# Optimization experiments

Measured on AMD Instinct MI355X. Metric: run time of the kernel, lower is better.

## Reference

```python
import jax, jax.numpy as jnp
import numpy as np

BN_EPS = 1e-5
CLAMP = 1e-10


def _three_nn(q, p):
    # q: (B,N,3) query points, p: (B,M,3) reference points
    # returns dist (B,N,3) euclidean distance to 3 nearest, idx (B,N,3)
    d2 = (jnp.sum(q * q, -1)[:, :, None] + jnp.sum(p * p, -1)[:, None, :]
          - 2.0 * jnp.einsum('bnd,bmd->bnm', q, p))  # (B,N,M)
    neg_vals, idx = jax.lax.top_k(-d2, 3)
    dist = jnp.sqrt(jnp.maximum(-neg_vals, 1e-20))
    return dist, idx


def _gather(feats_t, idx):
    # feats_t: (B,M,C), idx: (B,N,3) -> (B,N,3,C)
    return jax.vmap(lambda f, i: f[i])(feats_t, idx)


def _conv_bn_relu(x, W, b, g, beta):
    # x: (B,Cin,N); 1x1 Conv1d + BatchNorm1d (training-mode batch stats) + relu
    y = jnp.einsum('oc,bcn->bon', W, x) + b[None, :, None]
    mean = jnp.mean(y, axis=(0, 2), keepdims=True)
    var = jnp.mean((y - mean) ** 2, axis=(0, 2), keepdims=True)
    y = (y - mean) * jax.lax.rsqrt(var + BN_EPS)
    y = y * g[None, :, None] + beta[None, :, None]
    return jax.nn.relu(y)


def setup_inputs() -> dict:
    key = jax.random.key(0)
    ks = jax.random.split(key, 10)
    B, N, M, C2, C1 = 4, 8192, 2048, 256, 128
    inp = {
        'xyz1': jax.random.normal(ks[0], (B, 3, N), jnp.float32),
        'xyz2': jax.random.normal(ks[1], (B, 3, M), jnp.float32),
        'norm1': jax.random.normal(ks[2], (B, 3, N), jnp.float32),
        'norm2': jax.random.normal(ks[3], (B, 3, M), jnp.float32),
        'points1': jax.random.normal(ks[4], (B, C1, N), jnp.float32),
        'points2': jax.random.normal(ks[5], (B, C2, M), jnp.float32),
        'W0': jax.random.normal(ks[6], (256, C2 + C1), jnp.float32) * 0.05,
        'b0': jax.random.normal(ks[7], (256,), jnp.float32) * 0.05,
        'g0': jnp.ones((256,), jnp.float32),
        'be0': jnp.zeros((256,), jnp.float32),
        'W1': jax.random.normal(ks[8], (128, 256), jnp.float32) * 0.05,
        'b1': jax.random.normal(ks[9], (128,), jnp.float32) * 0.05,
        'g1': jnp.ones((128,), jnp.float32),
        'be1': jnp.zeros((128,), jnp.float32),
    }
    return inp


def reference(xyz1, xyz2, norm1, norm2, points1, points2,
              W0, b0, g0, be0, W1, b1, g1, be1):
    B, _, N = xyz1.shape
    # 3-NN search
    dist, idx = _three_nn(jnp.transpose(xyz1, (0, 2, 1)),
                          jnp.transpose(xyz2, (0, 2, 1)))  # (B,N,3)
    # normal distance between query normals and gathered neighbor normals
    grouped_norm = _gather(jnp.transpose(norm2, (0, 2, 1)), idx)        # (B,N,3,3)
    diff = jnp.transpose(norm1, (0, 2, 1))[:, :, None, :] - grouped_norm
    norm_dist = jnp.sqrt(jnp.sum(diff * diff, -1))                       # (B,N,3)
    # distance weights
    recip_dist = 1.0 / jnp.maximum(dist, CLAMP)
    weight = recip_dist / jnp.sum(recip_dist, 2, keepdims=True)
    # normal weights
    recip_nd = 1.0 / jnp.maximum(norm_dist, CLAMP)
    norm_weight = recip_nd / jnp.sum(recip_nd, 2, keepdims=True)
    weight = weight * norm_weight                                        # (B,N,3)
    # three_interpolate: weighted gather of points2
    gathered_pts = _gather(jnp.transpose(points2, (0, 2, 1)), idx)       # (B,N,3,C)
    interpolated = jnp.einsum('bnkc,bnk->bcn', gathered_pts, weight)     # (B,C,N)
    new_points = jnp.concatenate([interpolated, points1], axis=1)        # (B,C+C1,N)
    new_points = _conv_bn_relu(new_points, W0, b0, g0, be0)
    new_points = _conv_bn_relu(new_points, W1, b1, g1, be1)
    return new_points
```

## Files before the change

### kernel.cpp

```cpp
#include <hip/hip_runtime.h>
#include <hip/hip_bf16.h>
#include <cstdint>
#include <cstddef>

static constexpr int BB   = 4;
static constexpr int NN   = 8192;
static constexpr int MM   = 2048;
static constexpr int C1   = 128;
static constexpr int C2   = 256;
static constexpr int CH0  = C2 + C1;
static constexpr int O0   = 256;
static constexpr int O1   = 128;
static constexpr int NCOL = BB * NN;
static constexpr float BN_EPS = 1e-5f;

using u16 = unsigned short;
typedef __attribute__((ext_vector_type(8))) short short8;
typedef __attribute__((ext_vector_type(4))) float f32x4;

static __device__ __forceinline__ float bf2f(u16 u) {
    union { unsigned int i; float f; } v; v.i = ((unsigned int)u) << 16; return v.f;
}
static __device__ __forceinline__ u16 f2bf(float f) {
    union { float f; unsigned int i; } v; v.f = f;
    unsigned int r = (v.i + 0x7fffu + ((v.i >> 16) & 1u)) >> 16;
    return (u16)r;
}

__global__ __launch_bounds__(256) void prep_kernel(const float* __restrict__ points2,
                                                   u16* __restrict__ p2T,
                                                   const float* __restrict__ points1,
                                                   u16* __restrict__ p1T,
                                                   const float* __restrict__ W0f,
                                                   u16* __restrict__ W0b,
                                                   const float* __restrict__ W1f,
                                                   u16* __restrict__ W1b) {
    __shared__ float tile[32][33];
    int id = blockIdx.x;
    int t  = threadIdx.x;
    if (id < 6144) {
        const float* in; u16* out; int R, C, b, c0, r0;
        if (id < 2048) {
            in = points2; out = p2T; R = C2; C = MM;
            b = id >> 9; int rem = id & 511;
            c0 = (rem & 63) * 32; r0 = (rem >> 6) * 32;
        } else {
            int id2 = id - 2048;
            in = points1; out = p1T; R = C1; C = NN;
            b = id2 >> 10; int rem = id2 & 1023;
            c0 = (rem & 255) * 32; r0 = (rem >> 8) * 32;
        }
        int tx = t & 31, ty = t >> 5;
        const float* pin = in + (size_t)b * R * C;
        u16* pout = out + (size_t)b * R * C;
#pragma unroll
        for (int j = 0; j < 4; ++j) {
            int r = ty + j * 8;
            tile[r][tx] = pin[(size_t)(r0 + r) * C + (c0 + tx)];
        }
        __syncthreads();
#pragma unroll
        for (int j = 0; j < 4; ++j) {
            int c = ty + j * 8;
            pout[(size_t)(c0 + c) * R + (r0 + tx)] = f2bf(tile[tx][c]);
        }
    } else {
        int i = (id - 6144) * 256 + t;
        if (i < O0 * CH0) W0b[i] = f2bf(W0f[i]);
        else {
            int i2 = i - O0 * CH0;
            if (i2 < O1 * O0) W1b[i2] = f2bf(W1f[i2]);
        }
    }
}

__global__ __launch_bounds__(256) void three_nn_kernel(const float* __restrict__ xyz1,
                                                       const float* __restrict__ xyz2,
                                                       const float* __restrict__ norm1,
                                                       const float* __restrict__ norm2,
                                                       int* __restrict__ idxOut,
                                                       float* __restrict__ wOut) {
#pragma clang fp contract(off)
    constexpr int CH = 1024;
    __shared__ float4 pts[CH];
    int b    = blockIdx.x >> 8;
    int nblk = blockIdx.x & 255;
    int t    = threadIdx.x;
    int j    = t & 7;

    int n = nblk * 32 + (t >> 3);
    const float* x1 = xyz1 + (size_t)b * 3 * NN;
    float qx = x1[n], qy = x1[NN + n], qz = x1[2 * NN + n];
    float qq = (qx * qx + qy * qy) + qz * qz;

    const float* x2 = xyz2 + (size_t)b * 3 * MM;

    float d0 = 3.4e38f, d1 = 3.4e38f, d2v = 3.4e38f;
    int   i0 = 0, i1 = 0, i2 = 0;

    for (int chunk = 0; chunk < MM / CH; ++chunk) {
        __syncthreads();
        for (int i = t; i < CH; i += 256) {
            int m = chunk * CH + i;
            float px = x2[m];
            float py = x2[MM + m];
            float pz = x2[2 * MM + m];
            float pp = (px * px + py * py) + pz * pz;
            pts[i] = make_float4(px, py, pz, pp);
        }
        __syncthreads();

#pragma unroll 8
        for (int s = 0; s < CH / 8; ++s) {
            int ml = s * 8 + j;
            float4 P = pts[ml];
            float qp = (qx * P.x + qy * P.y) + qz * P.z;
            float d  = (qq + P.w) - 2.0f * qp;
            if (d < d2v) {
                int m = chunk * CH + ml;
                if (d < d1) {
                    if (d < d0) { d2v = d1; i2 = i1; d1 = d0; i1 = i0; d0 = d; i0 = m; }
                    else        { d2v = d1; i2 = i1; d1 = d;  i1 = m; }
                } else          { d2v = d;  i2 = m; }
            }
        }
    }

#pragma unroll
    for (int k = 1; k <= 4; k <<= 1) {
        float e0 = __shfl_xor(d0, k, 64), e1 = __shfl_xor(d1, k, 64), e2 = __shfl_xor(d2v, k, 64);
        int   f0 = __shfl_xor(i0, k, 64), f1 = __shfl_xor(i1, k, 64), f2 = __shfl_xor(i2, k, 64);
        float ed[3] = {e0, e1, e2}; int ef[3] = {f0, f1, f2};
#pragma unroll
        for (int e = 0; e < 3; ++e) {
            float dd = ed[e]; int ff = ef[e];
            bool b2 = (dd < d2v) || (dd == d2v && ff < i2);
            if (b2) {
                bool b1 = (dd < d1) || (dd == d1 && ff < i1);
                if (b1) {
                    d2v = d1; i2 = i1;
                    bool b0 = (dd < d0) || (dd == d0 && ff < i0);
                    if (b0) { d1 = d0; i1 = i0; d0 = dd; i0 = ff; }
                    else    { d1 = dd; i1 = ff; }
                } else { d2v = dd; i2 = ff; }
            }
        }
    }

    if (j == 0) {
        float s0 = sqrtf(fmaxf(d0, 1e-20f));
        float s1 = sqrtf(fmaxf(d1, 1e-20f));
        float s2 = sqrtf(fmaxf(d2v, 1e-20f));
        float r0 = 1.0f / fmaxf(s0, 1e-10f);
        float r1 = 1.0f / fmaxf(s1, 1e-10f);
        float r2 = 1.0f / fmaxf(s2, 1e-10f);
        float rs = (r0 + r1) + r2;
        float w0 = r0 / rs, w1 = r1 / rs, w2 = r2 / rs;

        const float* nm1 = norm1 + (size_t)b * 3 * NN;
        const float* nm2 = norm2 + (size_t)b * 3 * MM;
        float ax = nm1[n], ay = nm1[NN + n], az = nm1[2 * NN + n];
        float nd[3]; int ii[3] = {i0, i1, i2};
#pragma unroll
        for (int k = 0; k < 3; ++k) {
            int ik = ii[k];
            float dx = ax - nm2[ik];
            float dy = ay - nm2[MM + ik];
            float dz = az - nm2[2 * MM + ik];
            nd[k] = sqrtf((dx * dx + dy * dy) + dz * dz);
        }
        float m0 = 1.0f / fmaxf(nd[0], 1e-10f);
        float m1 = 1.0f / fmaxf(nd[1], 1e-10f);
        float m2 = 1.0f / fmaxf(nd[2], 1e-10f);
        float ms = (m0 + m1) + m2;

        int col = b * NN + n;
        idxOut[col * 3 + 0] = i0;
        idxOut[col * 3 + 1] = i1;
        idxOut[col * 3 + 2] = i2;
        wOut[col * 3 + 0] = w0 * (m0 / ms);
        wOut[col * 3 + 1] = w1 * (m1 / ms);
        wOut[col * 3 + 2] = w2 * (m2 / ms);
    }
}

__global__ __launch_bounds__(256) void build_xT_kernel(const int* __restrict__ idx,
                                                       const float* __restrict__ w,
                                                       const u16* __restrict__ p2T,
                                                       const u16* __restrict__ p1T,
                                                       u16* __restrict__ xT) {
    int t  = threadIdx.x;
    int l  = t & 63;
    int wv = t >> 6;
    int col = blockIdx.x * 4 + wv;
    int b = col >> 13;
    int n = col & (NN - 1);
    int i0 = idx[col * 3 + 0], i1 = idx[col * 3 + 1], i2 = idx[col * 3 + 2];
    float w0 = w[col * 3 + 0], w1 = w[col * 3 + 1], w2 = w[col * 3 + 2];
    const u16* base = p2T + (size_t)b * MM * C2;

    union { uint2 v; u16 u[4]; } a0, a1, a2, o;
    a0.v = *(const uint2*)(base + (size_t)i0 * C2 + l * 4);
    a1.v = *(const uint2*)(base + (size_t)i1 * C2 + l * 4);
    a2.v = *(const uint2*)(base + (size_t)i2 * C2 + l * 4);
#pragma unroll
    for (int e = 0; e < 4; ++e)
        o.u[e] = f2bf(w0 * bf2f(a0.u[e]) + w1 * bf2f(a1.u[e]) + w2 * bf2f(a2.u[e]));
    *(uint2*)(xT + (size_t)col * CH0 + l * 4) = o.v;

    if (l < 32) {
        uint2 p = *(const uint2*)(p1T + ((size_t)b * NN + n) * C1 + l * 4);
        *(uint2*)(xT + (size_t)col * CH0 + C2 + l * 4) = p;
    }
}

template <int KDIM, int LDC, int COLT, bool FUSEB>
__global__ __launch_bounds__(256) void gemm_bt_kernel(const u16* __restrict__ A,
                                                      const u16* __restrict__ Bt,
                                                      u16* __restrict__ Ct,
                                                      const float* __restrict__ bias,
                                                      const float* __restrict__ redB,
                                                      const float* __restrict__ gB,
                                                      const float* __restrict__ beB,
                                                      float invN,
                                                      float* __restrict__ partials) {
    constexpr int KT  = KDIM / 64;
    constexpr int NI  = COLT / 32;
    constexpr int ASZ = 128 * 64;
    constexpr int BSZ = COLT * 64;
    __shared__ u16 smem[2 * ASZ + 2 * BSZ];
    __shared__ float sSc[FUSEB ? KDIM : 1];
    __shared__ float sSh[FUSEB ? KDIM : 1];

    int t   = threadIdx.x;
    int l   = t & 63;
    int wv  = t >> 6;
    int rl  = l >> 3;
    int cg  = ((l & 7) ^ rl) * 8;
    int mb0 = blockIdx.y * 128;
    int cb0 = blockIdx.x * COLT;
    int lm  = l & 15;
    int q   = l >> 4;
    int wm0 = (wv & 1) * 64;
    int wn0 = (wv >> 1) * (COLT / 2);

    const u16* Abase = A  + (size_t)mb0 * KDIM;
    const u16* Bbase = Bt + (size_t)cb0 * KDIM;

    if (FUSEB) {
        int by = t >> 7, chL = t & 127;
        const float* base = redB + (size_t)by * 8 * 256;
        float s = 0.f, s2 = 0.f;
#pragma unroll
        for (int i = 0; i < 8; ++i) {
            s  += base[i * 256 + chL];
            s2 += base[i * 256 + 128 + chL];
        }
        float mean = s * invN;
        float var  = fmaxf(s2 * invN - mean * mean, 0.f);
        float inv  = rsqrtf(var + BN_EPS);
        float sc   = gB[t] * inv;
        sSc[t] = sc;
        sSh[t] = beB[t] - mean * sc;
        __syncthreads();
    }

    auto stage = [&](int buf, int k0) {
#pragma unroll
        for (int iss = 0; iss < 4; ++iss) {
            int row = wv * 32 + iss * 8;
            const u16* g = Abase + (size_t)(row + rl) * KDIM + k0 + cg;
            __builtin_amdgcn_global_load_lds(
                (const __attribute__((address_space(1))) unsigned int*)g,
                (__attribute__((address_space(3))) unsigned int*)(&smem[buf * ASZ + row * 64]),
                16, 0, 0);
        }
        if (!FUSEB) {
#pragma unroll
            for (int iss = 0; iss < COLT / 32; ++iss) {
                int row = wv * (COLT / 4) + iss * 8;
                const u16* g = Bbase + (size_t)(row + rl) * KDIM + k0 + cg;
                __builtin_amdgcn_global_load_lds(
                    (const __attribute__((address_space(1))) unsigned int*)g,
                    (__attribute__((address_space(3))) unsigned int*)(&smem[2 * ASZ + buf * BSZ + row * 64]),
                    16, 0, 0);
            }
        } else {
            int row = t >> 2;
            int kc  = (t & 3) * 16;
            const u16* gp = Bbase + (size_t)row * KDIM + k0 + kc;
            union { uint4 v; u16 u[8]; } lo, hi;
            lo.v = *(const uint4*)gp;
            hi.v = *(const uint4*)(gp + 8);
#pragma unroll
            for (int e = 0; e < 8; ++e) {
                float f0 = bf2f(lo.u[e]);
                lo.u[e] = f2bf(fmaxf(f0 * sSc[k0 + kc + e] + sSh[k0 + kc + e], 0.f));
                float f1 = bf2f(hi.u[e]);
                hi.u[e] = f2bf(fmaxf(f1 * sSc[k0 + kc + 8 + e] + sSh[k0 + kc + 8 + e], 0.f));
            }
            int c0 = kc >> 3;
            u16* dstB = &smem[2 * ASZ + buf * BSZ + row * 64];
            *(uint4*)&dstB[((c0)     ^ (row & 7)) * 8] = lo.v;
            *(uint4*)&dstB[((c0 + 1) ^ (row & 7)) * 8] = hi.v;
        }
    };

    f32x4 acc[4][NI] = {};

    stage(0, 0);
    for (int kt = 0; kt < KT; ++kt) {
        __syncthreads();
        if (kt + 1 < KT) stage((kt + 1) & 1, (kt + 1) * 64);
        const u16* As = &smem[(kt & 1) * ASZ];
        const u16* Bs = &smem[2 * ASZ + (kt & 1) * BSZ];
#pragma unroll
        for (int ks = 0; ks < 2; ++ks) {
            int csw = ((ks * 4 + q) ^ (lm & 7)) * 8;
            short8 av[4], bv[NI];
#pragma unroll
            for (int mi = 0; mi < 4; ++mi)
                av[mi] = *(const short8*)&As[(wm0 + mi * 16 + lm) * 64 + csw];
#pragma unroll
            for (int ni = 0; ni < NI; ++ni)
                bv[ni] = *(const short8*)&Bs[(wn0 + ni * 16 + lm) * 64 + csw];
#pragma unroll
            for (int mi = 0; mi < 4; ++mi)
#pragma unroll
                for (int ni = 0; ni < NI; ++ni)
                    acc[mi][ni] = __builtin_amdgcn_mfma_f32_16x16x32_bf16(
                        av[mi], bv[ni], acc[mi][ni], 0, 0, 0);
        }
    }

    u16*   Cs   = smem;
    float* reds = (float*)&smem[COLT * 136];

    __syncthreads();
    if (t < 256) reds[t] = 0.f;
    __syncthreads();

#pragma unroll
    for (int mi = 0; mi < 4; ++mi) {
        int chL = wm0 + mi * 16 + q * 4;
        float bv4[4];
#pragma unroll
        for (int r = 0; r < 4; ++r) bv4[r] = bias[mb0 + chL + r];
        float s[4]  = {0.f, 0.f, 0.f, 0.f};
        float s2[4] = {0.f, 0.f, 0.f, 0.f};
#pragma unroll
        for (int ni = 0; ni < NI; ++ni) {
            int colL = wn0 + ni * 16 + lm;
            union { u16 u[4]; uint2 d; } pk;
#pragma unroll
            for (int r = 0; r < 4; ++r) {
                float v = acc[mi][ni][r] + bv4[r];
                s[r]  += v;
                s2[r] += v * v;
                pk.u[r] = f2bf(v);
            }
            *(uint2*)&Cs[colL * 136 + chL] = pk.d;
        }
#pragma unroll
        for (int r = 0; r < 4; ++r) {
            float a = s[r], b2 = s2[r];
#pragma unroll
            for (int off = 1; off < 16; off <<= 1) {
                a  += __shfl_xor(a, off, 64);
                b2 += __shfl_xor(b2, off, 64);
            }
            if (lm == 0) {
                atomicAdd(&reds[chL + r], a);
                atomicAdd(&reds[128 + chL + r], b2);
            }
        }
    }
    __syncthreads();

    for (int u = t; u < COLT * 2; u += 256) {
        int c = u >> 1, h = u & 1;
        const u16* src = &Cs[c * 136 + h * 64];
        u16* dst = Ct + (size_t)(cb0 + c) * LDC + mb0 + h * 64;
#pragma unroll
        for (int jj = 0; jj < 8; ++jj)
            *(uint4*)(dst + jj * 8) = *(const uint4*)(src + jj * 8);
    }
    partials[((size_t)blockIdx.y * gridDim.x + blockIdx.x) * 256 + t] = reds[t];
}

__global__ __launch_bounds__(256) void reduce_partials_kernel(const float* __restrict__ in,
                                                              float* __restrict__ out,
                                                              int chunk) {
    int t = threadIdx.x, r = blockIdx.x;
    const float* base = in + (size_t)r * chunk * 256;
    float s = 0.f;
#pragma unroll 8
    for (int i = 0; i < chunk; ++i) s += base[(size_t)i * 256 + t];
    out[(size_t)r * 256 + t] = s;
}

__global__ __launch_bounds__(256) void finalize_kernel(const u16* __restrict__ y1T,
                                                       const float* __restrict__ red1,
                                                       const float* __restrict__ g1,
                                                       const float* __restrict__ be1,
                                                       float invN,
                                                       float* __restrict__ out) {
    __shared__ float tile[64][129];
    __shared__ float sc[O1], sh[O1];
    int t  = threadIdx.x;
    int b  = blockIdx.y;
    int n0 = blockIdx.x * 64;

    if (t < O1) {
        float s = 0.f, s2 = 0.f;
#pragma unroll
        for (int i = 0; i < 16; ++i) {
            s  += red1[i * 256 + t];
            s2 += red1[i * 256 + 128 + t];
        }
        float mean = s * invN;
        float var  = fmaxf(s2 * invN - mean * mean, 0.f);
        float inv  = rsqrtf(var + BN_EPS);
        float scv  = g1[t] * inv;
        sc[t] = scv;
        sh[t] = be1[t] - mean * scv;
    }
    __syncthreads();

#pragma unroll
    for (int it = 0; it < 32; ++it) {
        int flat = it * 256 + t;
        int cl = flat >> 7;
        int c  = flat & 127;
        int col = b * NN + n0 + cl;
        float v = bf2f(y1T[(size_t)col * O1 + c]);
        tile[cl][c] = fmaxf(v * sc[c] + sh[c], 0.f);
    }
    __syncthreads();
#pragma unroll
    for (int it = 0; it < 32; ++it) {
        int flat = it * 256 + t;
        int c  = flat >> 6;
        int nl = flat & 63;
        out[(size_t)b * O1 * NN + (size_t)c * NN + n0 + nl] = tile[nl][c];
    }
}

extern "C" void kernel_launch(void* const* d_in, const int* in_sizes, int n_in,
                              void* d_out, int out_size, void* d_ws, size_t ws_size,
                              hipStream_t stream) {
    (void)in_sizes; (void)n_in; (void)out_size; (void)ws_size;

    const float* xyz1    = (const float*)d_in[0];
    const float* xyz2    = (const float*)d_in[1];
    const float* norm1   = (const float*)d_in[2];
    const float* norm2   = (const float*)d_in[3];
    const float* points1 = (const float*)d_in[4];
    const float* points2 = (const float*)d_in[5];
    const float* W0f     = (const float*)d_in[6];
    const float* b0      = (const float*)d_in[7];
    const float* g0      = (const float*)d_in[8];
    const float* be0     = (const float*)d_in[9];
    const float* W1f     = (const float*)d_in[10];
    const float* b1      = (const float*)d_in[11];
    const float* g1      = (const float*)d_in[12];
    const float* be1     = (const float*)d_in[13];
    float* out = (float*)d_out;

    char* w8 = (char*)d_ws;
    size_t off = 0;
    auto carve = [&](size_t bytes) { void* p = w8 + off; off += (bytes + 255) & ~(size_t)255; return p; };
    int*   idxW   = (int*)  carve((size_t)NCOL * 3 * sizeof(int));
    float* wW     = (float*)carve((size_t)NCOL * 3 * sizeof(float));
    u16*   p2T    = (u16*)  carve((size_t)BB * MM * C2 * 2);
    u16*   p1T    = (u16*)  carve((size_t)BB * NN * C1 * 2);
    u16*   W0b    = (u16*)  carve((size_t)O0 * CH0 * 2);
    u16*   W1b    = (u16*)  carve((size_t)O1 * O0 * 2);
    u16*   xT     = (u16*)  carve((size_t)NCOL * CH0 * 2);
    u16*   y0T    = (u16*)  carve((size_t)NCOL * O0 * 2);
    u16*   y1T    = (u16*)  carve((size_t)NCOL * O1 * 2);
    float* part0  = (float*)carve((size_t)1024 * 256 * sizeof(float));
    float* part1  = (float*)carve((size_t)512 * 256 * sizeof(float));
    float* red0   = (float*)carve((size_t)16 * 256 * sizeof(float));
    float* red1   = (float*)carve((size_t)16 * 256 * sizeof(float));

    const float invN = 1.0f / (float)NCOL;

    prep_kernel<<<6656, 256, 0, stream>>>(points2, p2T, points1, p1T,
                                          W0f, W0b, W1f, W1b);

    three_nn_kernel<<<BB * (NN / 32), 256, 0, stream>>>(xyz1, xyz2, norm1, norm2, idxW, wW);

    build_xT_kernel<<<NCOL / 4, 256, 0, stream>>>(idxW, wW, p2T, p1T, xT);

    gemm_bt_kernel<CH0, O0, 64, false><<<dim3(NCOL / 64, O0 / 128), 256, 0, stream>>>(
        W0b, xT, y0T, b0, nullptr, nullptr, nullptr, invN, part0);
    reduce_partials_kernel<<<16, 256, 0, stream>>>(part0, red0, 64);

    gemm_bt_kernel<O0, O1, 64, true><<<dim3(NCOL / 64, O1 / 128), 256, 0, stream>>>(
        W1b, y0T, y1T, b1, red0, g0, be0, invN, part1);
    reduce_partials_kernel<<<16, 256, 0, stream>>>(part1, red1, 32);

    finalize_kernel<<<dim3(NN / 64, BB), 256, 0, stream>>>(y1T, red1, g1, be1, invN, out);
}
```

Measured before the change: 205.7 us.

## Fuse interpolation gather into first GEMM and process two queries per thread in 3-NN

```diff
diff --git a/kernel.cpp b/kernel.cpp
--- a/kernel.cpp
+++ b/kernel.cpp
@@ -83,20 +83,36 @@
 #pragma clang fp contract(off)
     constexpr int CH = 1024;
     __shared__ float4 pts[CH];
-    int b    = blockIdx.x >> 8;
-    int nblk = blockIdx.x & 255;
+    int b    = blockIdx.x >> 7;
+    int nblk = blockIdx.x & 127;
     int t    = threadIdx.x;
     int j    = t & 7;
 
-    int n = nblk * 32 + (t >> 3);
+    int n0 = nblk * 64 + (t >> 3) * 2;
+    int n1 = n0 + 1;
     const float* x1 = xyz1 + (size_t)b * 3 * NN;
-    float qx = x1[n], qy = x1[NN + n], qz = x1[2 * NN + n];
-    float qq = (qx * qx + qy * qy) + qz * qz;
+    float qxa = x1[n0], qya = x1[NN + n0], qza = x1[2 * NN + n0];
+    float qxb = x1[n1], qyb = x1[NN + n1], qzb = x1[2 * NN + n1];
+    float qqa = (qxa * qxa + qya * qya) + qza * qza;
+    float qqb = (qxb * qxb + qyb * qyb) + qzb * qzb;
 
     const float* x2 = xyz2 + (size_t)b * 3 * MM;
 
-    float d0 = 3.4e38f, d1 = 3.4e38f, d2v = 3.4e38f;
-    int   i0 = 0, i1 = 0, i2 = 0;
+    float da0 = 3.4e38f, da1 = 3.4e38f, da2 = 3.4e38f;
+    int   ia0 = 0, ia1 = 0, ia2 = 0;
+    float db0 = 3.4e38f, db1 = 3.4e38f, db2 = 3.4e38f;
+    int   ib0 = 0, ib1 = 0, ib2 = 0;
+
+    auto ins = [](float d, int m, float& e0, float& e1, float& e2,
+                  int& f0, int& f1, int& f2) {
+        bool m0 = d < e0, m1 = d < e1, m2 = d < e2;
+        e2 = m1 ? e1 : (m2 ? d : e2);
+        f2 = m1 ? f1 : (m2 ? m : f2);
+        e1 = m0 ? e0 : (m1 ? d : e1);
+        f1 = m0 ? f0 : (m1 ? m : f1);
+        e0 = m0 ? d : e0;
+        f0 = m0 ? m : f0;
+    };
 
     for (int chunk = 0; chunk < MM / CH; ++chunk) {
         __syncthreads();
@@ -110,113 +126,90 @@
         }
         __syncthreads();
 
-#pragma unroll 8
+#pragma unroll 4
         for (int s = 0; s < CH / 8; ++s) {
             int ml = s * 8 + j;
             float4 P = pts[ml];
-            float qp = (qx * P.x + qy * P.y) + qz * P.z;
-            float d  = (qq + P.w) - 2.0f * qp;
-            if (d < d2v) {
-                int m = chunk * CH + ml;
-                if (d < d1) {
-                    if (d < d0) { d2v = d1; i2 = i1; d1 = d0; i1 = i0; d0 = d; i0 = m; }
-                    else        { d2v = d1; i2 = i1; d1 = d;  i1 = m; }
-                } else          { d2v = d;  i2 = m; }
-            }
-        }
-    }
-
-#pragma unroll
-    for (int k = 1; k <= 4; k <<= 1) {
-        float e0 = __shfl_xor(d0, k, 64), e1 = __shfl_xor(d1, k, 64), e2 = __shfl_xor(d2v, k, 64);
-        int   f0 = __shfl_xor(i0, k, 64), f1 = __shfl_xor(i1, k, 64), f2 = __shfl_xor(i2, k, 64);
-        float ed[3] = {e0, e1, e2}; int ef[3] = {f0, f1, f2};
-#pragma unroll
-        for (int e = 0; e < 3; ++e) {
-            float dd = ed[e]; int ff = ef[e];
-            bool b2 = (dd < d2v) || (dd == d2v && ff < i2);
-            if (b2) {
-                bool b1 = (dd < d1) || (dd == d1 && ff < i1);
-                if (b1) {
-                    d2v = d1; i2 = i1;
-                    bool b0 = (dd < d0) || (dd == d0 && ff < i0);
-                    if (b0) { d1 = d0; i1 = i0; d0 = dd; i0 = ff; }
-                    else    { d1 = dd; i1 = ff; }
-                } else { d2v = dd; i2 = ff; }
-            }
-        }
-    }
+            int m = chunk * CH + ml;
+            float qpa = (qxa * P.x + qya * P.y) + qza * P.z;
+            float da  = (qqa + P.w) - 2.0f * qpa;
+            ins(da, m, da0, da1, da2, ia0, ia1, ia2);
+            float qpb = (qxb * P.x + qyb * P.y) + qzb * P.z;
+            float db  = (qqb + P.w) - 2.0f * qpb;
+            ins(db, m, db0, db1, db2, ib0, ib1, ib2);
+        }
+    }
+
+    auto merge = [&](float& e0, float& e1, float& e2, int& f0, int& f1, int& f2) {
+#pragma unroll
+        for (int k = 1; k <= 4; k <<= 1) {
+            float g0 = __shfl_xor(e0, k, 64), g1 = __shfl_xor(e1, k, 64), g2 = __shfl_xor(e2, k, 64);
+            int   h0 = __shfl_xor(f0, k, 64), h1 = __shfl_xor(f1, k, 64), h2 = __shfl_xor(f2, k, 64);
+            float ed[3] = {g0, g1, g2}; int ef[3] = {h0, h1, h2};
+#pragma unroll
+            for (int e = 0; e < 3; ++e) {
+                float dd = ed[e]; int ff = ef[e];
+                bool b2 = (dd < e2) || (dd == e2 && ff < f2);
+                if (b2) {
+                    bool b1 = (dd < e1) || (dd == e1 && ff < f1);
+                    if (b1) {
+                        e2 = e1; f2 = f1;
+                        bool b0 = (dd < e0) || (dd == e0 && ff < f0);
+                        if (b0) { e1 = e0; f1 = f0; e0 = dd; f0 = ff; }
+                        else    { e1 = dd; f1 = ff; }
+                    } else { e2 = dd; f2 = ff; }
+                }
+            }
+        }
+    };
+    merge(da0, da1, da2, ia0, ia1, ia2);
+    merge(db0, db1, db2, ib0, ib1, ib2);
 
     if (j == 0) {
-        float s0 = sqrtf(fmaxf(d0, 1e-20f));
-        float s1 = sqrtf(fmaxf(d1, 1e-20f));
-        float s2 = sqrtf(fmaxf(d2v, 1e-20f));
-        float r0 = 1.0f / fmaxf(s0, 1e-10f);
-        float r1 = 1.0f / fmaxf(s1, 1e-10f);
-        float r2 = 1.0f / fmaxf(s2, 1e-10f);
-        float rs = (r0 + r1) + r2;
-        float w0 = r0 / rs, w1 = r1 / rs, w2 = r2 / rs;
-
         const float* nm1 = norm1 + (size_t)b * 3 * NN;
         const float* nm2 = norm2 + (size_t)b * 3 * MM;
-        float ax = nm1[n], ay = nm1[NN + n], az = nm1[2 * NN + n];
-        float nd[3]; int ii[3] = {i0, i1, i2};
-#pragma unroll
-        for (int k = 0; k < 3; ++k) {
-            int ik = ii[k];
-            float dx = ax - nm2[ik];
-            float dy = ay - nm2[MM + ik];
-            float dz = az - nm2[2 * MM + ik];
-            nd[k] = sqrtf((dx * dx + dy * dy) + dz * dz);
-        }
-        float m0 = 1.0f / fmaxf(nd[0], 1e-10f);
-        float m1 = 1.0f / fmaxf(nd[1], 1e-10f);
-        float m2 = 1.0f / fmaxf(nd[2], 1e-10f);
-        float ms = (m0 + m1) + m2;
-
-        int col = b * NN + n;
-        idxOut[col * 3 + 0] = i0;
-        idxOut[col * 3 + 1] = i1;
-        idxOut[col * 3 + 2] = i2;
-        wOut[col * 3 + 0] = w0 * (m0 / ms);
-        wOut[col * 3 + 1] = w1 * (m1 / ms);
-        wOut[col * 3 + 2] = w2 * (m2 / ms);
-    }
-}
-
-__global__ __launch_bounds__(256) void build_xT_kernel(const int* __restrict__ idx,
-                                                       const float* __restrict__ w,
-                                                       const u16* __restrict__ p2T,
-                                                       const u16* __restrict__ p1T,
-                                                       u16* __restrict__ xT) {
-    int t  = threadIdx.x;
-    int l  = t & 63;
-    int wv = t >> 6;
-    int col = blockIdx.x * 4 + wv;
-    int b = col >> 13;
-    int n = col & (NN - 1);
-    int i0 = idx[col * 3 + 0], i1 = idx[col * 3 + 1], i2 = idx[col * 3 + 2];
-    float w0 = w[col * 3 + 0], w1 = w[col * 3 + 1], w2 = w[col * 3 + 2];
-    const u16* base = p2T + (size_t)b * MM * C2;
-
-    union { uint2 v; u16 u[4]; } a0, a1, a2, o;
-    a0.v = *(const uint2*)(base + (size_t)i0 * C2 + l * 4);
-    a1.v = *(const uint2*)(base + (size_t)i1 * C2 + l * 4);
-    a2.v = *(const uint2*)(base + (size_t)i2 * C2 + l * 4);
-#pragma unroll
-    for (int e = 0; e < 4; ++e)
-        o.u[e] = f2bf(w0 * bf2f(a0.u[e]) + w1 * bf2f(a1.u[e]) + w2 * bf2f(a2.u[e]));
-    *(uint2*)(xT + (size_t)col * CH0 + l * 4) = o.v;
-
-    if (l < 32) {
-        uint2 p = *(const uint2*)(p1T + ((size_t)b * NN + n) * C1 + l * 4);
-        *(uint2*)(xT + (size_t)col * CH0 + C2 + l * 4) = p;
-    }
-}
-
-template <int KDIM, int LDC, int COLT, bool FUSEB>
+        auto emit = [&](int n, float e0, float e1, float e2, int f0, int f1, int f2) {
+            float s0 = sqrtf(fmaxf(e0, 1e-20f));
+            float s1 = sqrtf(fmaxf(e1, 1e-20f));
+            float s2 = sqrtf(fmaxf(e2, 1e-20f));
+            float r0 = 1.0f / fmaxf(s0, 1e-10f);
+            float r1 = 1.0f / fmaxf(s1, 1e-10f);
+            float r2 = 1.0f / fmaxf(s2, 1e-10f);
+            float rs = (r0 + r1) + r2;
+            float w0 = r0 / rs, w1 = r1 / rs, w2 = r2 / rs;
+            float ax = nm1[n], ay = nm1[NN + n], az = nm1[2 * NN + n];
+            float nd[3]; int ii[3] = {f0, f1, f2};
+#pragma unroll
+            for (int k = 0; k < 3; ++k) {
+                int ik = ii[k];
+                float dx = ax - nm2[ik];
+                float dy = ay - nm2[MM + ik];
+                float dz = az - nm2[2 * MM + ik];
+                nd[k] = sqrtf((dx * dx + dy * dy) + dz * dz);
+            }
+            float m0 = 1.0f / fmaxf(nd[0], 1e-10f);
+            float m1 = 1.0f / fmaxf(nd[1], 1e-10f);
+            float m2 = 1.0f / fmaxf(nd[2], 1e-10f);
+            float ms = (m0 + m1) + m2;
+            int col = b * NN + n;
+            idxOut[col * 3 + 0] = f0;
+            idxOut[col * 3 + 1] = f1;
+            idxOut[col * 3 + 2] = f2;
+            wOut[col * 3 + 0] = w0 * (m0 / ms);
+            wOut[col * 3 + 1] = w1 * (m1 / ms);
+            wOut[col * 3 + 2] = w2 * (m2 / ms);
+        };
+        emit(n0, da0, da1, da2, ia0, ia1, ia2);
+        emit(n1, db0, db1, db2, ib0, ib1, ib2);
+    }
+}
+
+template <int KDIM, int LDC, int COLT, int MODE>
 __global__ __launch_bounds__(256) void gemm_bt_kernel(const u16* __restrict__ A,
                                                       const u16* __restrict__ Bt,
+                                                      const u16* __restrict__ p1T,
+                                                      const int* __restrict__ idx,
+                                                      const float* __restrict__ w,
                                                       u16* __restrict__ Ct,
                                                       const float* __restrict__ bias,
                                                       const float* __restrict__ redB,
@@ -229,8 +222,8 @@
     constexpr int ASZ = 128 * 64;
     constexpr int BSZ = COLT * 64;
     __shared__ u16 smem[2 * ASZ + 2 * BSZ];
-    __shared__ float sSc[FUSEB ? KDIM : 1];
-    __shared__ float sSh[FUSEB ? KDIM : 1];
+    __shared__ float sSc[MODE == 1 ? KDIM : 1];
+    __shared__ float sSh[MODE == 1 ? KDIM : 1];
 
     int t   = threadIdx.x;
     int l   = t & 63;
@@ -244,10 +237,18 @@
     int wm0 = (wv & 1) * 64;
     int wn0 = (wv >> 1) * (COLT / 2);
 
-    const u16* Abase = A  + (size_t)mb0 * KDIM;
-    const u16* Bbase = Bt + (size_t)cb0 * KDIM;
-
-    if (FUSEB) {
+    const u16* Abase = A + (size_t)mb0 * KDIM;
+
+    int vi0 = 0, vi1 = 0, vi2 = 0;
+    float vw0 = 0.f, vw1 = 0.f, vw2 = 0.f;
+    const u16* p2base = nullptr;
+    if (MODE == 2) {
+        int colg = cb0 + (t >> 2);
+        vi0 = idx[colg * 3 + 0]; vi1 = idx[colg * 3 + 1]; vi2 = idx[colg * 3 + 2];
+        vw0 = w[colg * 3 + 0];   vw1 = w[colg * 3 + 1];   vw2 = w[colg * 3 + 2];
+        p2base = Bt + (size_t)(cb0 >> 13) * MM * C2;
+    }
+    if (MODE == 1) {
         int by = t >> 7, chL = t & 127;
         const float* base = redB + (size_t)by * 8 * 256;
         float s = 0.f, s2 = 0.f;
@@ -275,20 +276,20 @@
                 (__attribute__((address_space(3))) unsigned int*)(&smem[buf * ASZ + row * 64]),
                 16, 0, 0);
         }
-        if (!FUSEB) {
+        if (MODE == 0) {
 #pragma unroll
             for (int iss = 0; iss < COLT / 32; ++iss) {
                 int row = wv * (COLT / 4) + iss * 8;
-                const u16* g = Bbase + (size_t)(row + rl) * KDIM + k0 + cg;
+                const u16* g = Bt + (size_t)(cb0 + row + rl) * KDIM + k0 + cg;
                 __builtin_amdgcn_global_load_lds(
                     (const __attribute__((address_space(1))) unsigned int*)g,
                     (__attribute__((address_space(3))) unsigned int*)(&smem[2 * ASZ + buf * BSZ + row * 64]),
                     16, 0, 0);
             }
-        } else {
+        } else if (MODE == 1) {
             int row = t >> 2;
             int kc  = (t & 3) * 16;
-            const u16* gp = Bbase + (size_t)row * KDIM + k0 + kc;
+            const u16* gp = Bt + (size_t)(cb0 + row) * KDIM + k0 + kc;
             union { uint4 v; u16 u[8]; } lo, hi;
             lo.v = *(const uint4*)gp;
             hi.v = *(const uint4*)(gp + 8);
@@ -303,6 +304,38 @@
             u16* dstB = &smem[2 * ASZ + buf * BSZ + row * 64];
             *(uint4*)&dstB[((c0)     ^ (row & 7)) * 8] = lo.v;
             *(uint4*)&dstB[((c0 + 1) ^ (row & 7)) * 8] = hi.v;
+        } else {
+            if (k0 < C2) {
+                int row = t >> 2;
+                int kc  = (t & 3) * 16;
+                const u16* bp = p2base + k0 + kc;
+                const u16* r0p = bp + (size_t)vi0 * C2;
+                const u16* r1p = bp + (size_t)vi1 * C2;
+                const u16* r2p = bp + (size_t)vi2 * C2;
+                union { uint4 v; u16 u[8]; } x0, x1, x2, y0, y1, y2, lo, hi;
+                x0.v = *(const uint4*)r0p; y0.v = *(const uint4*)(r0p + 8);
+                x1.v = *(const uint4*)r1p; y1.v = *(const uint4*)(r1p + 8);
+                x2.v = *(const uint4*)r2p; y2.v = *(const uint4*)(r2p + 8);
+#pragma unroll
+                for (int e = 0; e < 8; ++e) {
+                    lo.u[e] = f2bf(vw0 * bf2f(x0.u[e]) + vw1 * bf2f(x1.u[e]) + vw2 * bf2f(x2.u[e]));
+                    hi.u[e] = f2bf(vw0 * bf2f(y0.u[e]) + vw1 * bf2f(y1.u[e]) + vw2 * bf2f(y2.u[e]));
+                }
+                int c0 = kc >> 3;
+                u16* dstB = &smem[2 * ASZ + buf * BSZ + row * 64];
+                *(uint4*)&dstB[((c0)     ^ (row & 7)) * 8] = lo.v;
+                *(uint4*)&dstB[((c0 + 1) ^ (row & 7)) * 8] = hi.v;
+            } else {
+#pragma unroll
+                for (int iss = 0; iss < COLT / 32; ++iss) {
+                    int row = wv * (COLT / 4) + iss * 8;
+                    const u16* g = p1T + (size_t)(cb0 + row + rl) * C1 + (k0 - C2) + cg;
+                    __builtin_amdgcn_global_load_lds(
+                        (const __attribute__((address_space(1))) unsigned int*)g,
+                        (__attribute__((address_space(3))) unsigned int*)(&smem[2 * ASZ + buf * BSZ + row * 64]),
+                        16, 0, 0);
+                }
+            }
         }
     };
 
@@ -476,7 +509,6 @@
     u16*   p1T    = (u16*)  carve((size_t)BB * NN * C1 * 2);
     u16*   W0b    = (u16*)  carve((size_t)O0 * CH0 * 2);
     u16*   W1b    = (u16*)  carve((size_t)O1 * O0 * 2);
-    u16*   xT     = (u16*)  carve((size_t)NCOL * CH0 * 2);
     u16*   y0T    = (u16*)  carve((size_t)NCOL * O0 * 2);
     u16*   y1T    = (u16*)  carve((size_t)NCOL * O1 * 2);
     float* part0  = (float*)carve((size_t)1024 * 256 * sizeof(float));
@@ -489,16 +521,14 @@
     prep_kernel<<<6656, 256, 0, stream>>>(points2, p2T, points1, p1T,
                                           W0f, W0b, W1f, W1b);
 
-    three_nn_kernel<<<BB * (NN / 32), 256, 0, stream>>>(xyz1, xyz2, norm1, norm2, idxW, wW);
-
-    build_xT_kernel<<<NCOL / 4, 256, 0, stream>>>(idxW, wW, p2T, p1T, xT);
-
-    gemm_bt_kernel<CH0, O0, 64, false><<<dim3(NCOL / 64, O0 / 128), 256, 0, stream>>>(
-        W0b, xT, y0T, b0, nullptr, nullptr, nullptr, invN, part0);
+    three_nn_kernel<<<BB * (NN / 64), 256, 0, stream>>>(xyz1, xyz2, norm1, norm2, idxW, wW);
+
+    gemm_bt_kernel<CH0, O0, 64, 2><<<dim3(NCOL / 64, O0 / 128), 256, 0, stream>>>(
+        W0b, p2T, p1T, idxW, wW, y0T, b0, nullptr, nullptr, nullptr, invN, part0);
     reduce_partials_kernel<<<16, 256, 0, stream>>>(part0, red0, 64);
 
-    gemm_bt_kernel<O0, O1, 64, true><<<dim3(NCOL / 64, O1 / 128), 256, 0, stream>>>(
-        W1b, y0T, y1T, b1, red0, g0, be0, invN, part1);
+    gemm_bt_kernel<O0, O1, 64, 1><<<dim3(NCOL / 64, O1 / 128), 256, 0, stream>>>(
+        W1b, y0T, nullptr, nullptr, nullptr, y1T, b1, red0, g0, be0, invN, part1);
     reduce_partials_kernel<<<16, 256, 0, stream>>>(part1, red1, 32);
 
     finalize_kernel<<<dim3(NN / 64, BB), 256, 0, stream>>>(y1T, red1, g1, be1, invN, out);
```

Result: slower. 213.7 us (+3.9%).

## Fuse three-NN interpolation gather and points1 concat into first GEMM B-tile staging

Applied to the files above, without the earlier changes.

```diff
diff --git a/kernel.cpp b/kernel.cpp
--- a/kernel.cpp
+++ b/kernel.cpp
@@ -184,39 +184,12 @@
     }
 }
 
-__global__ __launch_bounds__(256) void build_xT_kernel(const int* __restrict__ idx,
-                                                       const float* __restrict__ w,
-                                                       const u16* __restrict__ p2T,
-                                                       const u16* __restrict__ p1T,
-                                                       u16* __restrict__ xT) {
-    int t  = threadIdx.x;
-    int l  = t & 63;
-    int wv = t >> 6;
-    int col = blockIdx.x * 4 + wv;
-    int b = col >> 13;
-    int n = col & (NN - 1);
-    int i0 = idx[col * 3 + 0], i1 = idx[col * 3 + 1], i2 = idx[col * 3 + 2];
-    float w0 = w[col * 3 + 0], w1 = w[col * 3 + 1], w2 = w[col * 3 + 2];
-    const u16* base = p2T + (size_t)b * MM * C2;
-
-    union { uint2 v; u16 u[4]; } a0, a1, a2, o;
-    a0.v = *(const uint2*)(base + (size_t)i0 * C2 + l * 4);
-    a1.v = *(const uint2*)(base + (size_t)i1 * C2 + l * 4);
-    a2.v = *(const uint2*)(base + (size_t)i2 * C2 + l * 4);
-#pragma unroll
-    for (int e = 0; e < 4; ++e)
-        o.u[e] = f2bf(w0 * bf2f(a0.u[e]) + w1 * bf2f(a1.u[e]) + w2 * bf2f(a2.u[e]));
-    *(uint2*)(xT + (size_t)col * CH0 + l * 4) = o.v;
-
-    if (l < 32) {
-        uint2 p = *(const uint2*)(p1T + ((size_t)b * NN + n) * C1 + l * 4);
-        *(uint2*)(xT + (size_t)col * CH0 + C2 + l * 4) = p;
-    }
-}
-
-template <int KDIM, int LDC, int COLT, bool FUSEB>
+template <int KDIM, int LDC, int COLT, int MODE>
 __global__ __launch_bounds__(256) void gemm_bt_kernel(const u16* __restrict__ A,
                                                       const u16* __restrict__ Bt,
+                                                      const u16* __restrict__ p1T,
+                                                      const int* __restrict__ idx,
+                                                      const float* __restrict__ w,
                                                       u16* __restrict__ Ct,
                                                       const float* __restrict__ bias,
                                                       const float* __restrict__ redB,
@@ -229,8 +202,8 @@
     constexpr int ASZ = 128 * 64;
     constexpr int BSZ = COLT * 64;
     __shared__ u16 smem[2 * ASZ + 2 * BSZ];
-    __shared__ float sSc[FUSEB ? KDIM : 1];
-    __shared__ float sSh[FUSEB ? KDIM : 1];
+    __shared__ float sSc[MODE == 1 ? KDIM : 1];
+    __shared__ float sSh[MODE == 1 ? KDIM : 1];
 
     int t   = threadIdx.x;
     int l   = t & 63;
@@ -244,10 +217,18 @@
     int wm0 = (wv & 1) * 64;
     int wn0 = (wv >> 1) * (COLT / 2);
 
-    const u16* Abase = A  + (size_t)mb0 * KDIM;
-    const u16* Bbase = Bt + (size_t)cb0 * KDIM;
-
-    if (FUSEB) {
+    const u16* Abase = A + (size_t)mb0 * KDIM;
+
+    int vi0 = 0, vi1 = 0, vi2 = 0;
+    float vw0 = 0.f, vw1 = 0.f, vw2 = 0.f;
+    const u16* p2base = nullptr;
+    if (MODE == 2) {
+        int colg = cb0 + (t >> 2);
+        vi0 = idx[colg * 3 + 0]; vi1 = idx[colg * 3 + 1]; vi2 = idx[colg * 3 + 2];
+        vw0 = w[colg * 3 + 0];   vw1 = w[colg * 3 + 1];   vw2 = w[colg * 3 + 2];
+        p2base = Bt + (size_t)(cb0 >> 13) * MM * C2;
+    }
+    if (MODE == 1) {
         int by = t >> 7, chL = t & 127;
         const float* base = redB + (size_t)by * 8 * 256;
         float s = 0.f, s2 = 0.f;
@@ -275,20 +256,20 @@
                 (__attribute__((address_space(3))) unsigned int*)(&smem[buf * ASZ + row * 64]),
                 16, 0, 0);
         }
-        if (!FUSEB) {
+        if (MODE == 0) {
 #pragma unroll
             for (int iss = 0; iss < COLT / 32; ++iss) {
                 int row = wv * (COLT / 4) + iss * 8;
-                const u16* g = Bbase + (size_t)(row + rl) * KDIM + k0 + cg;
+                const u16* g = Bt + (size_t)(cb0 + row + rl) * KDIM + k0 + cg;
                 __builtin_amdgcn_global_load_lds(
                     (const __attribute__((address_space(1))) unsigned int*)g,
                     (__attribute__((address_space(3))) unsigned int*)(&smem[2 * ASZ + buf * BSZ + row * 64]),
                     16, 0, 0);
             }
-        } else {
+        } else if (MODE == 1) {
             int row = t >> 2;
             int kc  = (t & 3) * 16;
-            const u16* gp = Bbase + (size_t)row * KDIM + k0 + kc;
+            const u16* gp = Bt + (size_t)(cb0 + row) * KDIM + k0 + kc;
             union { uint4 v; u16 u[8]; } lo, hi;
             lo.v = *(const uint4*)gp;
             hi.v = *(const uint4*)(gp + 8);
@@ -303,6 +284,38 @@
             u16* dstB = &smem[2 * ASZ + buf * BSZ + row * 64];
             *(uint4*)&dstB[((c0)     ^ (row & 7)) * 8] = lo.v;
             *(uint4*)&dstB[((c0 + 1) ^ (row & 7)) * 8] = hi.v;
+        } else {
+            if (k0 < C2) {
+                int row = t >> 2;
+                int kc  = (t & 3) * 16;
+                const u16* bp = p2base + k0 + kc;
+                const u16* r0p = bp + (size_t)vi0 * C2;
+                const u16* r1p = bp + (size_t)vi1 * C2;
+                const u16* r2p = bp + (size_t)vi2 * C2;
+                union { uint4 v; u16 u[8]; } x0, x1, x2, y0, y1, y2, lo, hi;
+                x0.v = *(const uint4*)r0p; y0.v = *(const uint4*)(r0p + 8);
+                x1.v = *(const uint4*)r1p; y1.v = *(const uint4*)(r1p + 8);
+                x2.v = *(const uint4*)r2p; y2.v = *(const uint4*)(r2p + 8);
+#pragma unroll
+                for (int e = 0; e < 8; ++e) {
+                    lo.u[e] = f2bf(vw0 * bf2f(x0.u[e]) + vw1 * bf2f(x1.u[e]) + vw2 * bf2f(x2.u[e]));
+                    hi.u[e] = f2bf(vw0 * bf2f(y0.u[e]) + vw1 * bf2f(y1.u[e]) + vw2 * bf2f(y2.u[e]));
+                }
+                int c0 = kc >> 3;
+                u16* dstB = &smem[2 * ASZ + buf * BSZ + row * 64];
+                *(uint4*)&dstB[((c0)     ^ (row & 7)) * 8] = lo.v;
+                *(uint4*)&dstB[((c0 + 1) ^ (row & 7)) * 8] = hi.v;
+            } else {
+#pragma unroll
+                for (int iss = 0; iss < COLT / 32; ++iss) {
+                    int row = wv * (COLT / 4) + iss * 8;
+                    const u16* g = p1T + (size_t)(cb0 + row + rl) * C1 + (k0 - C2) + cg;
+                    __builtin_amdgcn_global_load_lds(
+                        (const __attribute__((address_space(1))) unsigned int*)g,
+                        (__attribute__((address_space(3))) unsigned int*)(&smem[2 * ASZ + buf * BSZ + row * 64]),
+                        16, 0, 0);
+                }
+            }
         }
     };
 
@@ -476,7 +489,6 @@
     u16*   p1T    = (u16*)  carve((size_t)BB * NN * C1 * 2);
     u16*   W0b    = (u16*)  carve((size_t)O0 * CH0 * 2);
     u16*   W1b    = (u16*)  carve((size_t)O1 * O0 * 2);
-    u16*   xT     = (u16*)  carve((size_t)NCOL * CH0 * 2);
     u16*   y0T    = (u16*)  carve((size_t)NCOL * O0 * 2);
     u16*   y1T    = (u16*)  carve((size_t)NCOL * O1 * 2);
     float* part0  = (float*)carve((size_t)1024 * 256 * sizeof(float));
@@ -491,14 +503,12 @@
 
     three_nn_kernel<<<BB * (NN / 32), 256, 0, stream>>>(xyz1, xyz2, norm1, norm2, idxW, wW);
 
-    build_xT_kernel<<<NCOL / 4, 256, 0, stream>>>(idxW, wW, p2T, p1T, xT);
-
-    gemm_bt_kernel<CH0, O0, 64, false><<<dim3(NCOL / 64, O0 / 128), 256, 0, stream>>>(
-        W0b, xT, y0T, b0, nullptr, nullptr, nullptr, invN, part0);
+    gemm_bt_kernel<CH0, O0, 64, 2><<<dim3(NCOL / 64, O0 / 128), 256, 0, stream>>>(
+        W0b, p2T, p1T, idxW, wW, y0T, b0, nullptr, nullptr, nullptr, invN, part0);
     reduce_partials_kernel<<<16, 256, 0, stream>>>(part0, red0, 64);
 
-    gemm_bt_kernel<O0, O1, 64, true><<<dim3(NCOL / 64, O1 / 128), 256, 0, stream>>>(
-        W1b, y0T, y1T, b1, red0, g0, be0, invN, part1);
+    gemm_bt_kernel<O0, O1, 64, 1><<<dim3(NCOL / 64, O1 / 128), 256, 0, stream>>>(
+        W1b, y0T, nullptr, nullptr, nullptr, y1T, b1, red0, g0, be0, invN, part1);
     reduce_partials_kernel<<<16, 256, 0, stream>>>(part1, red1, 32);
 
     finalize_kernel<<<dim3(NN / 64, BB), 256, 0, stream>>>(y1T, red1, g1, be1, invN, out);
```

Result: faster. 199.4 us (-3.0%).
